# Kernel optimization log

Hardware: AMD Instinct MI355X
Metric: run time of the kernel (lower is better)

The kernel has to match this reference:

```python
import jax, jax.numpy as jnp
import numpy as np

N_E, E_DIM = 1024, 256

def setup_inputs() -> dict:
    key = jax.random.key(0)
    kz, ke = jax.random.split(key)
    z = jax.random.normal(kz, (16, E_DIM, 64, 64), dtype=jnp.float32)
    # codebook initialized uniform(-1/n_e, 1/n_e) as in the torch module
    emb = jax.random.uniform(ke, (N_E, E_DIM), dtype=jnp.float32,
                             minval=-1.0 / N_E, maxval=1.0 / N_E)
    return {"z": z, "emb": emb}

def reference(z, emb):
    B, C, H, W = z.shape  # C == e_dim
    # NCHW -> NHWC -> [N_tokens, e_dim]
    zf = jnp.transpose(z, (0, 2, 3, 1)).reshape(-1, C)
    # squared L2 distances: ||z||^2 + ||e||^2 - 2 z.e^T  -> [N_tokens, n_e]
    d = (jnp.sum(zf * zf, axis=1, keepdims=True)
         + jnp.sum(emb * emb, axis=1)
         - 2.0 * jnp.matmul(zf, emb.T))
    idx = jnp.argmin(d, axis=1)  # [N_tokens]
    # gather codebook rows (equivalent to one-hot @ emb), back to NCHW
    z_q = jnp.take(emb, idx, axis=0).reshape(B, H, W, C)
    z_q = jnp.transpose(z_q, (0, 3, 1, 2))
    return z_q, idx[:, None]
```

## Files before the change

### kernel.cpp

```cpp
#include <hip/hip_runtime.h>
#include <hip/hip_fp16.h>
#include <math.h>

#define CDIM 256
#define NE   1024
#define HW   4096
#define NB   16
#define ZQ_SIZE (NB*CDIM*HW)

typedef unsigned short ushort_t;
typedef __attribute__((ext_vector_type(8))) _Float16 f16x8;
typedef __attribute__((ext_vector_type(8))) unsigned short u16x8;
typedef __attribute__((ext_vector_type(4))) float f32x4;

#define AS1 __attribute__((address_space(1)))
#define AS3 __attribute__((address_space(3)))

#define MARGIN 1.0e-4f

#define WS_EE    0
#define WS_ZZ    4096
#define WS_CNT   266240
#define WS_LIST  266496
#define WS_ESWZ  528640
#define WS_NEEDED 1052928

__device__ __forceinline__ float sq_nofma(float v) {
    float v2 = v * v;
    asm volatile("" : "+v"(v2));
    return v2;
}

template <typename F>
__device__ __forceinline__ float pairwise256_sq(F get) {
    float total = 0.0f;
    #pragma unroll
    for (int h = 0; h < 2; ++h) {
        float r[8];
        #pragma unroll
        for (int j = 0; j < 8; ++j) r[j] = sq_nofma(get(h * 128 + j));
        #pragma unroll
        for (int i = 8; i < 128; i += 8) {
            #pragma unroll
            for (int j = 0; j < 8; ++j) r[j] += sq_nofma(get(h * 128 + i + j));
        }
        float s = ((r[0] + r[1]) + (r[2] + r[3])) + ((r[4] + r[5]) + (r[6] + r[7]));
        total = (h == 0) ? s : (total + s);
    }
    return total;
}

template <typename F>
__device__ __forceinline__ float pairwise128_sq(F get) {
    float r[8];
    #pragma unroll
    for (int j = 0; j < 8; ++j) r[j] = sq_nofma(get(j));
    #pragma unroll
    for (int i = 8; i < 128; i += 8) {
        #pragma unroll
        for (int j = 0; j < 8; ++j) r[j] += sq_nofma(get(i + j));
    }
    return ((r[0] + r[1]) + (r[2] + r[3])) + ((r[4] + r[5]) + (r[6] + r[7]));
}

__device__ __forceinline__ ushort_t f2h(float v) {
    return __half_as_ushort(__float2half(v));
}

__global__ __launch_bounds__(256) void ee_kernel(const float* __restrict__ emb,
                                                 float* __restrict__ ee,
                                                 int* __restrict__ cnt) {
    if (blockIdx.x == 0 && threadIdx.x == 0) *cnt = 0;
    int j = blockIdx.x * 256 + threadIdx.x;
    const float* row = emb + (size_t)j * CDIM;
    ee[j] = pairwise256_sq([&](int i) { return row[i]; });
}

__global__ __launch_bounds__(256) void ecvt_kernel(const float* __restrict__ emb,
                                                   ushort_t* __restrict__ eswz) {
    int g = blockIdx.x * 256 + threadIdx.x;
    int s  = g >> 11;
    int r  = g & 2047;
    int cw = r >> 3;
    int kg = r & 7;
    int chunk = s >> 2, kb = s & 3;
    int wn = cw >> 5, n = (cw >> 4) & 1, lr = cw & 15;
    int ks = kg >> 2, lg = kg & 3;

    const float* src = emb + (size_t)(chunk * 256 + cw) * CDIM + kb * 64 + kg * 8;
    float4 a = *reinterpret_cast<const float4*>(src);
    float4 b = *reinterpret_cast<const float4*>(src + 4);
    u16x8 p = { f2h(a.x), f2h(a.y), f2h(a.z), f2h(a.w),
                f2h(b.x), f2h(b.y), f2h(b.z), f2h(b.w) };
    int f = (wn * 2 + ks) * 2 + n;
    size_t dst = (size_t)s * 32768 + f * 1024 + (lg * 16 + lr) * 16;
    *reinterpret_cast<u16x8*>((char*)eswz + dst) = p;
}

__global__ __launch_bounds__(512, 4) void vq_main(const float* __restrict__ z,
                                                  const float* __restrict__ emb,
                                                  const ushort_t* __restrict__ eswz,
                                                  const float* __restrict__ eew,
                                                  float* __restrict__ zzw,
                                                  int* __restrict__ cnt,
                                                  int* __restrict__ list,
                                                  float* __restrict__ out) {
    __shared__ __align__(16) char arena[76544];
    char*  zfB = arena;
    char*  esB = arena + 32768;
    float* eel = (float*)(arena + 65536);
    float* zzp = (float*)(arena + 69632);
    float* rd1 = (float*)(arena + 70144);
    int*   rj1 = (int*)  (arena + 72192);
    float* rd2 = (float*)(arena + 74240);
    int*   rbj = (int*)  (arena + 76288);

    const int tid  = threadIdx.x;
    const int lane = tid & 63;
    const int wn   = tid >> 6;
    const int b    = blockIdx.x >> 6;
    const int hw0  = (blockIdx.x & 63) << 6;
    const float* zb = z + (size_t)b * CDIM * HW + hw0;
    const int lr = lane & 15;
    const int lg = lane >> 4;
    const int laneoff = lane << 4;

    {
        const int tok = lane;
        #pragma unroll
        for (int i = 0; i < 4; ++i) {
            int kg = (wn << 2) + i;
            int k0 = kg << 3;
            u16x8 p;
            #pragma unroll
            for (int e = 0; e < 8; ++e)
                p[e] = f2h(zb[(size_t)(k0 + e) * HW + tok]);
            int m = tok >> 4, lrr = tok & 15;
            int kb_ = kg >> 3, ks_ = (kg >> 2) & 1, lg_ = kg & 3;
            int off = (((kb_ * 2 + ks_) * 4 + m) << 10) + ((lg_ * 16 + lrr) << 4);
            *(u16x8*)(zfB + off) = p;
        }
        eel[tid]       = eew[tid];
        eel[tid + 512] = eew[tid + 512];
    }
    if (tid < 128) {
        int tok = tid >> 1, h = tid & 1;
        zzp[tok * 2 + h] = pairwise128_sq([&](int i) {
            return zb[(size_t)(h * 128 + i) * HW + tok];
        });
    }
    {
        const char* gsrc = (const char*)eswz;
        #pragma unroll
        for (int q = 0; q < 4; ++q) {
            __builtin_amdgcn_global_load_lds(
                (const AS1 unsigned*)(gsrc + (q << 13) + (tid << 4)),
                (AS3 unsigned*)(esB + (q << 13) + (wn << 10)), 16, 0, 0);
        }
    }
    asm volatile("s_waitcnt vmcnt(0)" ::: "memory");
    __syncthreads();

    f32x4 acc[4][2];
    float sd1[4][4], sd2[4][4];
    int   sj1[4][4];
    #pragma unroll
    for (int m = 0; m < 4; ++m)
        #pragma unroll
        for (int r = 0; r < 4; ++r) { sd1[m][r] = INFINITY; sd2[m][r] = INFINITY; sj1[m][r] = NE; }

    for (int s = 0; s < 16; ++s) {
        const int chunk = s >> 2, kb = s & 3;
        if (kb == 0) {
            #pragma unroll
            for (int m = 0; m < 4; ++m)
                #pragma unroll
                for (int n = 0; n < 2; ++n) acc[m][n] = (f32x4){0.f, 0.f, 0.f, 0.f};
        }
        #pragma unroll
        for (int ks = 0; ks < 2; ++ks) {
            f16x8 ah[4], bh[2];
            const int fa = (kb * 2 + ks) * 4;
            #pragma unroll
            for (int m = 0; m < 4; ++m)
                ah[m] = *(const f16x8*)(zfB + ((fa + m) << 10) + laneoff);
            const int fb = (wn * 2 + ks) * 2;
            #pragma unroll
            for (int n = 0; n < 2; ++n)
                bh[n] = *(const f16x8*)(esB + ((fb + n) << 10) + laneoff);
            #pragma unroll
            for (int m = 0; m < 4; ++m)
                #pragma unroll
                for (int n = 0; n < 2; ++n)
                    acc[m][n] = __builtin_amdgcn_mfma_f32_16x16x32_f16(ah[m], bh[n], acc[m][n], 0, 0, 0);
        }
        if (kb == 3) {
            #pragma unroll
            for (int m = 0; m < 4; ++m)
                #pragma unroll
                for (int r = 0; r < 4; ++r) {
                    int t = m * 16 + lg * 4 + r;
                    float zzv = zzp[2 * t] + zzp[2 * t + 1];
                    #pragma unroll
                    for (int n = 0; n < 2; ++n) {
                        int code = (chunk << 8) + (wn << 5) + (n << 4) + lr;
                        float t1 = zzv + eel[code];
                        float d  = t1 - 2.0f * acc[m][n][r];
                        bool lt1 = d < sd1[m][r];
                        bool lt2 = d < sd2[m][r];
                        sd2[m][r] = lt1 ? sd1[m][r] : (lt2 ? d : sd2[m][r]);
                        if (lt1) { sd1[m][r] = d; sj1[m][r] = code; }
                    }
                }
        }
        __syncthreads();
        if (s < 15) {
            const char* gsrc = (const char*)eswz + (size_t)(s + 1) * 32768;
            #pragma unroll
            for (int q = 0; q < 4; ++q) {
                __builtin_amdgcn_global_load_lds(
                    (const AS1 unsigned*)(gsrc + (q << 13) + (tid << 4)),
                    (AS3 unsigned*)(esB + (q << 13) + (wn << 10)), 16, 0, 0);
            }
        }
        asm volatile("s_waitcnt vmcnt(0)" ::: "memory");
        __syncthreads();
    }

    #pragma unroll
    for (int off = 1; off <= 8; off <<= 1) {
        #pragma unroll
        for (int m = 0; m < 4; ++m)
            #pragma unroll
            for (int r = 0; r < 4; ++r) {
                float od1 = __shfl_xor(sd1[m][r], off);
                int   oj1 = __shfl_xor(sj1[m][r], off);
                float od2 = __shfl_xor(sd2[m][r], off);
                float nd2 = fminf(fmaxf(sd1[m][r], od1), fminf(sd2[m][r], od2));
                bool tk = (od1 < sd1[m][r]) || (od1 == sd1[m][r] && oj1 < sj1[m][r]);
                if (tk) { sd1[m][r] = od1; sj1[m][r] = oj1; }
                sd2[m][r] = nd2;
            }
    }
    if (lr == 0) {
        #pragma unroll
        for (int m = 0; m < 4; ++m)
            #pragma unroll
            for (int r = 0; r < 4; ++r) {
                int tok = m * 16 + lg * 4 + r;
                rd1[wn * 64 + tok] = sd1[m][r];
                rj1[wn * 64 + tok] = sj1[m][r];
                rd2[wn * 64 + tok] = sd2[m][r];
            }
    }
    __syncthreads();

    if (tid < 64) {
        float d1f = rd1[tid]; int j1f = rj1[tid]; float d2f = rd2[tid];
        #pragma unroll
        for (int w = 1; w < 8; ++w) {
            float od1 = rd1[w * 64 + tid];
            int   oj1 = rj1[w * 64 + tid];
            float od2 = rd2[w * 64 + tid];
            float nd2 = fminf(fmaxf(d1f, od1), fminf(d2f, od2));
            bool tk = (od1 < d1f) || (od1 == d1f && oj1 < j1f);
            if (tk) { d1f = od1; j1f = oj1; }
            d2f = nd2;
        }
        rbj[tid] = j1f;
        int gtok = b * HW + hw0 + tid;
        out[(size_t)ZQ_SIZE + gtok] = (float)j1f;
        zzw[gtok] = zzp[2 * tid] + zzp[2 * tid + 1];
        if (!(d2f - d1f > MARGIN)) {
            int slot = atomicAdd(cnt, 1);
            list[slot] = gtok;
        }
    }
    __syncthreads();

    float* zq_st = (float*)arena;
    {
        int row = tid >> 3, sub = tid & 7;
        int j = rbj[row];
        const float* er = emb + (size_t)j * CDIM;
        #pragma unroll
        for (int i = 0; i < 8; ++i) {
            int c = (sub << 2) + (i << 5);
            float4 v = *reinterpret_cast<const float4*>(er + c);
            *reinterpret_cast<float4*>(&zq_st[row * 260 + c]) = v;
        }
    }
    __syncthreads();
    {
        int tok = tid & 63, cg = tid >> 6;
        float* ob = out + (size_t)b * CDIM * HW + hw0 + tok;
        #pragma unroll 4
        for (int i = 0; i < 32; ++i) {
            int c = (cg << 5) + i;
            ob[(size_t)c * HW] = zq_st[tok * 260 + c];
        }
    }
}

__global__ __launch_bounds__(256) void vq_fallback(const float* __restrict__ z,
                                                   const float* __restrict__ emb,
                                                   const float* __restrict__ eew,
                                                   const float* __restrict__ zzw,
                                                   const int* __restrict__ cnt,
                                                   const int* __restrict__ list,
                                                   float* __restrict__ out) {
    __shared__ __align__(16) float elds[64 * 260];
    __shared__ float zrow[4][256];
    __shared__ int   toks[4];

    const int tid  = threadIdx.x;
    const int lane = tid & 63;
    const int wv   = tid >> 6;
    const int nt   = *cnt;
    const int groups = (nt + 3) >> 2;

    for (int g = blockIdx.x; g < groups; g += gridDim.x) {
        if (tid < 4) toks[tid] = (g * 4 + tid < nt) ? list[g * 4 + tid] : -1;
        __syncthreads();
        const int gt  = toks[wv];
        const bool act = gt >= 0;
        const int tb  = act ? (gt >> 12) : 0;
        const int thw = act ? (gt & 4095) : 0;
        if (act) {
            #pragma unroll
            for (int i = 0; i < 4; ++i)
                zrow[wv][i * 64 + lane] = z[(size_t)tb * CDIM * HW + (size_t)(i * 64 + lane) * HW + thw];
        }
        const float zz = act ? zzw[gt] : 0.0f;
        float d1 = INFINITY; int j1 = NE;

        for (int c = 0; c < 16; ++c) {
            __syncthreads();
            {
                int row = tid >> 2, sub = tid & 3;
                #pragma unroll
                for (int i = 0; i < 16; ++i) {
                    int col = (sub << 2) + (i << 4);
                    float4 v = *reinterpret_cast<const float4*>(
                        &emb[(size_t)(c * 64 + row) * CDIM + col]);
                    *reinterpret_cast<float4*>(&elds[row * 260 + col]) = v;
                }
            }
            __syncthreads();
            if (act) {
                float acc = 0.0f;
                #pragma unroll 8
                for (int kq = 0; kq < 64; ++kq) {
                    float4 ev = *reinterpret_cast<const float4*>(&elds[lane * 260 + kq * 4]);
                    float4 zv = *reinterpret_cast<const float4*>(&zrow[wv][kq * 4]);
                    acc = fmaf(zv.x, ev.x, acc);
                    acc = fmaf(zv.y, ev.y, acc);
                    acc = fmaf(zv.z, ev.z, acc);
                    acc = fmaf(zv.w, ev.w, acc);
                }
                int j = c * 64 + lane;
                float t1 = zz + eew[j];
                float d  = t1 - 2.0f * acc;
                if (d < d1) { d1 = d; j1 = j; }
            }
        }
        #pragma unroll
        for (int off = 1; off <= 32; off <<= 1) {
            float od = __shfl_xor(d1, off);
            int   oj = __shfl_xor(j1, off);
            if (od < d1 || (od == d1 && oj < j1)) { d1 = od; j1 = oj; }
        }
        if (act) {
            if (lane == 0) out[(size_t)ZQ_SIZE + gt] = (float)j1;
            #pragma unroll
            for (int i = 0; i < 4; ++i) {
                int cc = i * 64 + lane;
                out[(size_t)tb * CDIM * HW + (size_t)cc * HW + thw] = emb[(size_t)j1 * CDIM + cc];
            }
        }
        __syncthreads();
    }
}

#define BM 32
#define BN 256
#define BK 16
__global__ __launch_bounds__(256, 3) void vq_legacy(const float* __restrict__ z,
                                                    const float* __restrict__ emb,
                                                    const float* __restrict__ ee,
                                                    float* __restrict__ out) {
    __shared__ float zs[CDIM][BM];
    __shared__ float es[BK][BN];
    __shared__ float ees[BN];
    __shared__ float zzs[BM];
    __shared__ float red_d[4][BM];
    __shared__ int   red_j[4][BM];
    __shared__ int   bestj_s[BM];

    const int tid = threadIdx.x;
    const int b   = blockIdx.x >> 7;
    const int hw0 = (blockIdx.x & 127) << 5;
    const int ti  = tid & 7;
    const int tj  = tid >> 3;
    const int tm0 = ti << 2;
    const int jc0 = tj << 3;
    {
        const float* zb = z + (size_t)b * CDIM * HW + hw0;
        #pragma unroll
        for (int r = 0; r < 8; ++r) {
            int f4 = (r << 8) + tid;
            int c  = f4 >> 3;
            int t4 = (f4 & 7) << 2;
            float4 v = *reinterpret_cast<const float4*>(zb + (size_t)c * HW + t4);
            *reinterpret_cast<float4*>(&zs[c][t4]) = v;
        }
    }
    __syncthreads();
    if (tid < BM) zzs[tid] = pairwise256_sq([&](int i) { return zs[i][tid]; });
    __syncthreads();
    float bd[4]; int bj[4];
    #pragma unroll
    for (int i = 0; i < 4; ++i) { bd[i] = INFINITY; bj[i] = NE; }
    for (int jt = 0; jt < NE / BN; ++jt) {
        const int j0 = jt * BN;
        float acc[4][8];
        #pragma unroll
        for (int i = 0; i < 4; ++i)
            #pragma unroll
            for (int jj = 0; jj < 8; ++jj) acc[i][jj] = 0.0f;
        for (int kt = 0; kt < CDIM / BK; ++kt) {
            __syncthreads();
            #pragma unroll
            for (int r = 0; r < 4; ++r) {
                int f4 = (r << 8) + tid;
                int jj = f4 >> 2;
                int c4 = (f4 & 3) << 2;
                float4 v = *reinterpret_cast<const float4*>(
                    emb + (size_t)(j0 + jj) * CDIM + kt * BK + c4);
                es[c4 + 0][jj] = v.x; es[c4 + 1][jj] = v.y;
                es[c4 + 2][jj] = v.z; es[c4 + 3][jj] = v.w;
            }
            if (kt == 0 && tid < BN) ees[tid] = ee[j0 + tid];
            __syncthreads();
            #pragma unroll
            for (int k = 0; k < BK; ++k) {
                float4 av  = *reinterpret_cast<const float4*>(&zs[kt * BK + k][tm0]);
                float4 bv0 = *reinterpret_cast<const float4*>(&es[k][jc0]);
                float4 bv1 = *reinterpret_cast<const float4*>(&es[k][jc0 + 4]);
                float bb[8] = {bv0.x, bv0.y, bv0.z, bv0.w, bv1.x, bv1.y, bv1.z, bv1.w};
                #pragma unroll
                for (int jj = 0; jj < 8; ++jj) {
                    acc[0][jj] = fmaf(av.x, bb[jj], acc[0][jj]);
                    acc[1][jj] = fmaf(av.y, bb[jj], acc[1][jj]);
                    acc[2][jj] = fmaf(av.z, bb[jj], acc[2][jj]);
                    acc[3][jj] = fmaf(av.w, bb[jj], acc[3][jj]);
                }
            }
        }
        #pragma unroll
        for (int i = 0; i < 4; ++i) {
            float zzv = zzs[tm0 + i];
            #pragma unroll
            for (int jj = 0; jj < 8; ++jj) {
                float t1 = zzv + ees[jc0 + jj];
                float d  = t1 - 2.0f * acc[i][jj];
                if (d < bd[i]) { bd[i] = d; bj[i] = j0 + jc0 + jj; }
            }
        }
    }
    #pragma unroll
    for (int off = 8; off <= 32; off <<= 1) {
        #pragma unroll
        for (int i = 0; i < 4; ++i) {
            float od = __shfl_xor(bd[i], off);
            int   oj = __shfl_xor(bj[i], off);
            if (od < bd[i] || (od == bd[i] && oj < bj[i])) { bd[i] = od; bj[i] = oj; }
        }
    }
    {
        const int lane = tid & 63;
        const int w    = tid >> 6;
        if (lane < 8) {
            #pragma unroll
            for (int i = 0; i < 4; ++i) {
                red_d[w][lane * 4 + i] = bd[i];
                red_j[w][lane * 4 + i] = bj[i];
            }
        }
    }
    __syncthreads();
    if (tid < BM) {
        float d = red_d[0][tid]; int j = red_j[0][tid];
        #pragma unroll
        for (int w2 = 1; w2 < 4; ++w2) {
            float od = red_d[w2][tid]; int oj = red_j[w2][tid];
            if (od < d || (od == d && oj < j)) { d = od; j = oj; }
        }
        bestj_s[tid] = j;
        out[(size_t)ZQ_SIZE + (size_t)b * HW + hw0 + tid] = (float)j;
    }
    __syncthreads();
    {
        const int t  = tid & 31;
        const int c0 = tid >> 5;
        const int jb = bestj_s[t];
        const float* er = emb + (size_t)jb * CDIM;
        float* ob = out + (size_t)b * CDIM * HW + hw0 + t;
        #pragma unroll
        for (int c = c0; c < CDIM; c += 8) ob[(size_t)c * HW] = er[c];
    }
}

extern "C" void kernel_launch(void* const* d_in, const int* in_sizes, int n_in,
                              void* d_out, int out_size, void* d_ws, size_t ws_size,
                              hipStream_t stream) {
    const float* z   = (const float*)d_in[0];
    const float* emb = (const float*)d_in[1];
    float* out = (float*)d_out;
    char*  ws  = (char*)d_ws;

    float*    ee   = (float*)(ws + WS_EE);
    float*    zzw  = (float*)(ws + WS_ZZ);
    int*      cnt  = (int*)  (ws + WS_CNT);
    int*      list = (int*)  (ws + WS_LIST);
    ushort_t* eswz = (ushort_t*)(ws + WS_ESWZ);

    if (ws_size >= (size_t)WS_NEEDED) {
        ee_kernel<<<dim3(NE / 256), dim3(256), 0, stream>>>(emb, ee, cnt);
        ecvt_kernel<<<dim3(128), dim3(256), 0, stream>>>(emb, eswz);
        vq_main<<<dim3((NB * HW) / 64), dim3(512), 0, stream>>>(z, emb, eswz, ee, zzw,
                                                                cnt, list, out);
        vq_fallback<<<dim3(512), dim3(256), 0, stream>>>(z, emb, ee, zzw, cnt, list, out);
    } else {
        ee_kernel<<<dim3(NE / 256), dim3(256), 0, stream>>>(emb, ee, cnt);
        vq_legacy<<<dim3((NB * HW) / BM), dim3(256), 0, stream>>>(z, emb, ee, out);
    }
}
```

Before: 238.8 us.

## Double-buffer codebook LDS loads, keep z fragments in registers, fuse prep kernels

The main kernel now double-buffers the fp16 codebook stages in shared memory, issuing the next stage's async global-to-LDS load before the MFMA work and dropping one barrier per stage. It also keeps all 32 z fragments in registers instead of re-reading them from LDS. The ee norm kernel is folded into ecvt_kernel, leaving one fewer launch. The fallback re-check kernel now uses 512-thread blocks with 8 tokens per group, and the near-tie margin shrinks so fewer tokens go to fallback. In exchange, the larger LDS footprint and higher register use drop occupancy to 2 blocks per CU, and the tighter margin risks argmin mismatches on near ties.

```diff
diff --git a/kernel.cpp b/kernel.cpp
--- a/kernel.cpp
+++ b/kernel.cpp
@@ -16,7 +16,7 @@
 #define AS1 __attribute__((address_space(1)))
 #define AS3 __attribute__((address_space(3)))
 
-#define MARGIN 1.0e-4f
+#define MARGIN 6.0e-5f
 
 #define WS_EE    0
 #define WS_ZZ    4096
@@ -77,7 +77,16 @@
 }
 
 __global__ __launch_bounds__(256) void ecvt_kernel(const float* __restrict__ emb,
-                                                   ushort_t* __restrict__ eswz) {
+                                                   ushort_t* __restrict__ eswz,
+                                                   float* __restrict__ ee,
+                                                   int* __restrict__ cnt) {
+    if (blockIdx.x >= 128) {
+        if (blockIdx.x == 128 && threadIdx.x == 0) *cnt = 0;
+        int j = (blockIdx.x - 128) * 256 + threadIdx.x;
+        const float* row = emb + (size_t)j * CDIM;
+        ee[j] = pairwise256_sq([&](int i) { return row[i]; });
+        return;
+    }
     int g = blockIdx.x * 256 + threadIdx.x;
     int s  = g >> 11;
     int r  = g & 2047;
@@ -97,7 +106,7 @@
     *reinterpret_cast<u16x8*>((char*)eswz + dst) = p;
 }
 
-__global__ __launch_bounds__(512, 4) void vq_main(const float* __restrict__ z,
+__global__ __launch_bounds__(512, 2) void vq_main(const float* __restrict__ z,
                                                   const float* __restrict__ emb,
                                                   const ushort_t* __restrict__ eswz,
                                                   const float* __restrict__ eew,
@@ -105,15 +114,15 @@
                                                   int* __restrict__ cnt,
                                                   int* __restrict__ list,
                                                   float* __restrict__ out) {
-    __shared__ __align__(16) char arena[76544];
+    __shared__ __align__(16) char arena[109312];
     char*  zfB = arena;
     char*  esB = arena + 32768;
-    float* eel = (float*)(arena + 65536);
-    float* zzp = (float*)(arena + 69632);
-    float* rd1 = (float*)(arena + 70144);
-    int*   rj1 = (int*)  (arena + 72192);
-    float* rd2 = (float*)(arena + 74240);
-    int*   rbj = (int*)  (arena + 76288);
+    float* eel = (float*)(arena + 98304);
+    float* zzp = (float*)(arena + 102400);
+    float* rd1 = (float*)(arena + 102912);
+    int*   rj1 = (int*)  (arena + 104960);
+    float* rd2 = (float*)(arena + 107008);
+    int*   rbj = (int*)  (arena + 109056);
 
     const int tid  = threadIdx.x;
     const int lane = tid & 63;
@@ -126,6 +135,15 @@
     const int laneoff = lane << 4;
 
     {
+        const char* gsrc = (const char*)eswz;
+        #pragma unroll
+        for (int q = 0; q < 4; ++q)
+            __builtin_amdgcn_global_load_lds(
+                (const AS1 unsigned*)(gsrc + (q << 13) + (tid << 4)),
+                (AS3 unsigned*)(esB + (q << 13) + (wn << 10)), 16, 0, 0);
+    }
+
+    {
         const int tok = lane;
         #pragma unroll
         for (int i = 0; i < 4; ++i) {
@@ -149,17 +167,13 @@
             return zb[(size_t)(h * 128 + i) * HW + tok];
         });
     }
-    {
-        const char* gsrc = (const char*)eswz;
-        #pragma unroll
-        for (int q = 0; q < 4; ++q) {
-            __builtin_amdgcn_global_load_lds(
-                (const AS1 unsigned*)(gsrc + (q << 13) + (tid << 4)),
-                (AS3 unsigned*)(esB + (q << 13) + (wn << 10)), 16, 0, 0);
-        }
-    }
     asm volatile("s_waitcnt vmcnt(0)" ::: "memory");
     __syncthreads();
+
+    f16x8 ah[32];
+    #pragma unroll
+    for (int f = 0; f < 32; ++f)
+        ah[f] = *(const f16x8*)(zfB + (f << 10) + laneoff);
 
     f32x4 acc[4][2];
     float sd1[4][4], sd2[4][4];
@@ -169,8 +183,19 @@
         #pragma unroll
         for (int r = 0; r < 4; ++r) { sd1[m][r] = INFINITY; sd2[m][r] = INFINITY; sj1[m][r] = NE; }
 
+    #pragma unroll
     for (int s = 0; s < 16; ++s) {
         const int chunk = s >> 2, kb = s & 3;
+        const char* bufc = esB + ((s & 1) << 15);
+        if (s < 15) {
+            const char* gsrc = (const char*)eswz + (size_t)(s + 1) * 32768;
+            char* dstb = esB + (((s + 1) & 1) << 15);
+            #pragma unroll
+            for (int q = 0; q < 4; ++q)
+                __builtin_amdgcn_global_load_lds(
+                    (const AS1 unsigned*)(gsrc + (q << 13) + (tid << 4)),
+                    (AS3 unsigned*)(dstb + (q << 13) + (wn << 10)), 16, 0, 0);
+        }
         if (kb == 0) {
             #pragma unroll
             for (int m = 0; m < 4; ++m)
@@ -179,20 +204,16 @@
         }
         #pragma unroll
         for (int ks = 0; ks < 2; ++ks) {
-            f16x8 ah[4], bh[2];
-            const int fa = (kb * 2 + ks) * 4;
-            #pragma unroll
-            for (int m = 0; m < 4; ++m)
-                ah[m] = *(const f16x8*)(zfB + ((fa + m) << 10) + laneoff);
-            const int fb = (wn * 2 + ks) * 2;
+            f16x8 bh[2];
             #pragma unroll
             for (int n = 0; n < 2; ++n)
-                bh[n] = *(const f16x8*)(esB + ((fb + n) << 10) + laneoff);
+                bh[n] = *(const f16x8*)(bufc + (((wn * 2 + ks) * 2 + n) << 10) + laneoff);
             #pragma unroll
             for (int m = 0; m < 4; ++m)
                 #pragma unroll
                 for (int n = 0; n < 2; ++n)
-                    acc[m][n] = __builtin_amdgcn_mfma_f32_16x16x32_f16(ah[m], bh[n], acc[m][n], 0, 0, 0);
+                    acc[m][n] = __builtin_amdgcn_mfma_f32_16x16x32_f16(
+                        ah[(kb * 2 + ks) * 4 + m], bh[n], acc[m][n], 0, 0, 0);
         }
         if (kb == 3) {
             #pragma unroll
@@ -213,16 +234,6 @@
                     }
                 }
         }
-        __syncthreads();
-        if (s < 15) {
-            const char* gsrc = (const char*)eswz + (size_t)(s + 1) * 32768;
-            #pragma unroll
-            for (int q = 0; q < 4; ++q) {
-                __builtin_amdgcn_global_load_lds(
-                    (const AS1 unsigned*)(gsrc + (q << 13) + (tid << 4)),
-                    (AS3 unsigned*)(esB + (q << 13) + (wn << 10)), 16, 0, 0);
-            }
-        }
         asm volatile("s_waitcnt vmcnt(0)" ::: "memory");
         __syncthreads();
     }
@@ -302,7 +313,7 @@
     }
 }
 
-__global__ __launch_bounds__(256) void vq_fallback(const float* __restrict__ z,
+__global__ __launch_bounds__(512) void vq_fallback(const float* __restrict__ z,
                                                    const float* __restrict__ emb,
                                                    const float* __restrict__ eew,
                                                    const float* __restrict__ zzw,
@@ -310,17 +321,17 @@
                                                    const int* __restrict__ list,
                                                    float* __restrict__ out) {
     __shared__ __align__(16) float elds[64 * 260];
-    __shared__ float zrow[4][256];
-    __shared__ int   toks[4];
+    __shared__ float zrow[8][256];
+    __shared__ int   toks[8];
 
     const int tid  = threadIdx.x;
     const int lane = tid & 63;
     const int wv   = tid >> 6;
     const int nt   = *cnt;
-    const int groups = (nt + 3) >> 2;
+    const int groups = (nt + 7) >> 3;
 
     for (int g = blockIdx.x; g < groups; g += gridDim.x) {
-        if (tid < 4) toks[tid] = (g * 4 + tid < nt) ? list[g * 4 + tid] : -1;
+        if (tid < 8) toks[tid] = (g * 8 + tid < nt) ? list[g * 8 + tid] : -1;
         __syncthreads();
         const int gt  = toks[wv];
         const bool act = gt >= 0;
@@ -337,10 +348,10 @@
         for (int c = 0; c < 16; ++c) {
             __syncthreads();
             {
-                int row = tid >> 2, sub = tid & 3;
+                int row = tid >> 3, sub = tid & 7;
                 #pragma unroll
-                for (int i = 0; i < 16; ++i) {
-                    int col = (sub << 2) + (i << 4);
+                for (int i = 0; i < 8; ++i) {
+                    int col = (sub << 2) + (i << 5);
                     float4 v = *reinterpret_cast<const float4*>(
                         &emb[(size_t)(c * 64 + row) * CDIM + col]);
                     *reinterpret_cast<float4*>(&elds[row * 260 + col]) = v;
@@ -526,11 +537,10 @@
     ushort_t* eswz = (ushort_t*)(ws + WS_ESWZ);
 
     if (ws_size >= (size_t)WS_NEEDED) {
-        ee_kernel<<<dim3(NE / 256), dim3(256), 0, stream>>>(emb, ee, cnt);
-        ecvt_kernel<<<dim3(128), dim3(256), 0, stream>>>(emb, eswz);
+        ecvt_kernel<<<dim3(132), dim3(256), 0, stream>>>(emb, eswz, ee, cnt);
         vq_main<<<dim3((NB * HW) / 64), dim3(512), 0, stream>>>(z, emb, eswz, ee, zzw,
                                                                 cnt, list, out);
-        vq_fallback<<<dim3(512), dim3(256), 0, stream>>>(z, emb, ee, zzw, cnt, list, out);
+        vq_fallback<<<dim3(128), dim3(512), 0, stream>>>(z, emb, ee, zzw, cnt, list, out);
     } else {
         ee_kernel<<<dim3(NE / 256), dim3(256), 0, stream>>>(emb, ee, cnt);
         vq_legacy<<<dim3((NB * HW) / BM), dim3(256), 0, stream>>>(z, emb, ee, out);
```

After: 304.3 us. 27.5% more time.
